# Optimization experiments

Hardware: AMD Instinct MI355X
Metric: run time of the kernel (lower is better)

The kernel has to match this reference:

```python
import jax, jax.numpy as jnp
import numpy as np

B, L, D, H, E, TOP_K = 8, 2048, 1024, 4096, 8, 2
TAU = 1.0
EPS = 1e-9


def setup_inputs() -> dict:
    key = jax.random.key(0)
    ks = jax.random.split(key, 8)
    T = B * L
    s = 0.02
    return {
        "x": jax.random.normal(ks[0], (B, L, D), dtype=jnp.float32),
        "snr": jax.random.uniform(ks[1], (1,), dtype=jnp.float32) * 10.0,
        "gumbel_u": jax.random.uniform(ks[2], (T, E), dtype=jnp.float32),
        "gate_w1": jax.random.normal(ks[3], (D + 1, D), dtype=jnp.float32) * s,
        "gate_b1": jnp.zeros((D,), dtype=jnp.float32),
        "gate_w2": jax.random.normal(ks[4], (D, E), dtype=jnp.float32) * s,
        "gate_b2": jnp.zeros((E,), dtype=jnp.float32),
        "ew1": jax.random.normal(ks[5], (E, D, H), dtype=jnp.float32) * s,
        "eb1": jnp.zeros((E, H), dtype=jnp.float32),
        "ew2": jax.random.normal(ks[6], (E, H, D), dtype=jnp.float32) * s,
        "eb2": jnp.zeros((E, D), dtype=jnp.float32),
    }


def reference(x, snr, gumbel_u, gate_w1, gate_b1, gate_w2, gate_b2, ew1, eb1, ew2, eb2):
    b, l, d = x.shape
    T = b * l
    xf = x.reshape(T, d)  # [T, D]

    # --- gate: Linear(D+1,D) -> ReLU -> Linear(D,E), snr appended per token ---
    g_in = jnp.concatenate([xf, jnp.broadcast_to(snr, (T, 1))], axis=-1)
    h = jax.nn.relu(g_in @ gate_w1 + gate_b1)
    logits = h @ gate_w2 + gate_b2  # [T, E]

    # --- gumbel softmax (soft, hard=False) ---
    gumbel = -jnp.log(-jnp.log(gumbel_u + EPS) + EPS)
    gate_scores = jax.nn.softmax((logits + gumbel) / TAU, axis=-1)  # [T, E]

    # --- top-k dispatch weights ---
    topk_scores, topk_idx = jax.lax.top_k(gate_scores, TOP_K)  # [T, K]
    onehot_k = jax.nn.one_hot(topk_idx, E, dtype=gate_scores.dtype)  # [T, K, E]
    comb = jnp.einsum("tk,tke->te", topk_scores, onehot_k)  # combine weights [T, E]
    expert_mask = onehot_k.sum(axis=1)  # [T, E], 1.0 where expert selected

    # --- per-expert FFN, weighted combine (dense over tokens per expert) ---
    out = jnp.zeros_like(xf)
    for e in range(E):
        he = jax.nn.relu(xf @ ew1[e] + eb1[e])  # [T, H]
        oe = he @ ew2[e] + eb2[e]  # [T, D]
        out = out + comb[:, e:e + 1] * oe

    return out.reshape(b, l, d), gate_scores, expert_mask
```

## Files before the change

kernel.cpp:

```cpp
#include <hip/hip_runtime.h>

typedef unsigned short u16;
typedef __attribute__((ext_vector_type(8))) short bf16x8;
typedef __attribute__((ext_vector_type(4))) float f32x4;

#define T_TOK 16384
#define DDIM  1024
#define HDIM  4096
#define NEXP  8
#define HC    2048

static constexpr size_t XBF_OFF  = 0;
static constexpr size_t EW1T_OFF = XBF_OFF  + (size_t)T_TOK*DDIM*2;
static constexpr size_t EW2T_OFF = EW1T_OFF + (size_t)NEXP*HDIM*DDIM*2;
static constexpr size_t TOK_OFF  = EW2T_OFF + (size_t)NEXP*DDIM*HDIM*2;
static constexpr size_t PICK_OFF = TOK_OFF  + (size_t)NEXP*T_TOK*4;
static constexpr size_t CNT_OFF  = PICK_OFF + (size_t)NEXP*T_TOK*4;
static constexpr size_t BASE_OFF = CNT_OFF  + 256;
static constexpr size_t BEFF_OFF = BASE_OFF + 256;
static constexpr size_t T2S_OFF  = BEFF_OFF + 4096;
static constexpr size_t T2W_OFF  = T2S_OFF  + (size_t)T_TOK*8;
static constexpr size_t OE_OFF   = T2W_OFF  + (size_t)T_TOK*8;
static constexpr size_t OE_ROWS  = 2*T_TOK + 128;
static constexpr size_t HBUF_OFF = OE_OFF + OE_ROWS*(size_t)DDIM*4;
static constexpr size_t WS_NEEDED = HBUF_OFF + OE_ROWS*(size_t)HC*2;
static constexpr size_t XLO_OFF  = HBUF_OFF;
static constexpr size_t W1HT_OFF = XLO_OFF + (size_t)T_TOK*DDIM*2;
static constexpr size_t W1LT_OFF = W1HT_OFF + (size_t)DDIM*DDIM*2;

__device__ __forceinline__ u16 f2bf(float f) {
  unsigned u = __float_as_uint(f);
  unsigned r = (u + 0x7FFFu + ((u >> 16) & 1u)) >> 16;
  return (u16)r;
}
__device__ __forceinline__ float bf2f(u16 b) { return __uint_as_float(((unsigned)b) << 16); }

#define GL16(gp, lp) __builtin_amdgcn_global_load_lds( \
    (const __attribute__((address_space(1))) void*)(gp), \
    (__attribute__((address_space(3))) void*)(lp), 16, 0, 0)

__global__ __launch_bounds__(256) void k_convert_x2(const float* __restrict__ x, u16* __restrict__ xh,
                                                    u16* __restrict__ xl, int n4) {
  int i = blockIdx.x * blockDim.x + threadIdx.x;
  int stride = gridDim.x * blockDim.x;
  for (; i < n4; i += stride) {
    float4 v = *(((const float4*)x) + i);
    u16 h0 = f2bf(v.x), h1 = f2bf(v.y), h2 = f2bf(v.z), h3 = f2bf(v.w);
    u16 l0 = f2bf(v.x - bf2f(h0)), l1 = f2bf(v.y - bf2f(h1));
    u16 l2 = f2bf(v.z - bf2f(h2)), l3 = f2bf(v.w - bf2f(h3));
    uint2 ph, pl;
    ph.x = (unsigned)h0 | ((unsigned)h1 << 16);
    ph.y = (unsigned)h2 | ((unsigned)h3 << 16);
    pl.x = (unsigned)l0 | ((unsigned)l1 << 16);
    pl.y = (unsigned)l2 | ((unsigned)l3 << 16);
    *(uint2*)(xh + (size_t)i * 4) = ph;
    *(uint2*)(xl + (size_t)i * 4) = pl;
  }
}

__global__ __launch_bounds__(256) void k_bias_eff(const float* __restrict__ w1, const float* __restrict__ b1,
                                                  const float* __restrict__ snr, float* __restrict__ beff) {
  int j = blockIdx.x * 256 + threadIdx.x;
  if (j < DDIM) beff[j] = b1[j] + snr[0] * w1[(size_t)DDIM * DDIM + j];
}

__global__ __launch_bounds__(256) void k_transpose_bf16(const float* __restrict__ in, u16* __restrict__ out,
                                                        int Rr, int Cc) {
  __shared__ u16 tile[64][72];
  const float* inE = in + (size_t)blockIdx.z * Rr * Cc;
  u16* outE = out + (size_t)blockIdx.z * Rr * Cc;
  int r0 = blockIdx.x * 64, c0 = blockIdx.y * 64;
  #pragma unroll
  for (int i = 0; i < 4; i++) {
    int id = threadIdx.x + i * 256;
    int r = id >> 4, cq = id & 15;
    float4 v = *(const float4*)(inE + (size_t)(r0 + r) * Cc + c0 + cq * 4);
    tile[cq*4+0][r] = f2bf(v.x);
    tile[cq*4+1][r] = f2bf(v.y);
    tile[cq*4+2][r] = f2bf(v.z);
    tile[cq*4+3][r] = f2bf(v.w);
  }
  __syncthreads();
  #pragma unroll
  for (int i = 0; i < 2; i++) {
    int id = threadIdx.x + i * 256;
    int c = id >> 3, rq = id & 7;
    *(uint4*)(outE + (size_t)(c0 + c) * Rr + r0 + rq * 8) = *(const uint4*)&tile[c][rq * 8];
  }
}

__global__ __launch_bounds__(256) void k_transpose_w1split(const float* __restrict__ w1,
                                                           u16* __restrict__ hT, u16* __restrict__ lT) {
  __shared__ u16 th[64][72];
  __shared__ u16 tl[64][72];
  int r0 = blockIdx.x * 64, c0 = blockIdx.y * 64;
  #pragma unroll
  for (int i = 0; i < 4; i++) {
    int id = threadIdx.x + i * 256;
    int r = id >> 4, cq = id & 15;
    float4 v = *(const float4*)(w1 + (size_t)(r0 + r) * DDIM + c0 + cq * 4);
    u16 h0 = f2bf(v.x), h1 = f2bf(v.y), h2 = f2bf(v.z), h3 = f2bf(v.w);
    th[cq*4+0][r] = h0; tl[cq*4+0][r] = f2bf(v.x - bf2f(h0));
    th[cq*4+1][r] = h1; tl[cq*4+1][r] = f2bf(v.y - bf2f(h1));
    th[cq*4+2][r] = h2; tl[cq*4+2][r] = f2bf(v.z - bf2f(h2));
    th[cq*4+3][r] = h3; tl[cq*4+3][r] = f2bf(v.w - bf2f(h3));
  }
  __syncthreads();
  #pragma unroll
  for (int i = 0; i < 2; i++) {
    int id = threadIdx.x + i * 256;
    int c = id >> 3, rq = id & 7;
    *(uint4*)(hT + (size_t)(c0 + c) * DDIM + r0 + rq * 8) = *(const uint4*)&th[c][rq * 8];
    *(uint4*)(lT + (size_t)(c0 + c) * DDIM + r0 + rq * 8) = *(const uint4*)&tl[c][rq * 8];
  }
}

#define MFMA_STEP(Abuf, Bbuf)                                                     \
  do {                                                                            \
    _Pragma("unroll")                                                             \
    for (int ks = 0; ks < 2; ks++) {                                              \
      const int chk = ks * 4 + (lane >> 4);                                       \
      bf16x8 af[4], bfr[4];                                                       \
      _Pragma("unroll")                                                           \
      for (int m = 0; m < 4; m++) {                                               \
        int row = wr + m * 16 + (lane & 15);                                      \
        af[m] = *(const bf16x8*)&(Abuf)[row * 64 + ((chk ^ (row & 7)) * 8)];      \
      }                                                                           \
      _Pragma("unroll")                                                           \
      for (int n = 0; n < 4; n++) {                                               \
        int col = wc + n * 16 + (lane & 15);                                      \
        bfr[n] = *(const bf16x8*)&(Bbuf)[col * 64 + ((chk ^ (col & 7)) * 8)];     \
      }                                                                           \
      _Pragma("unroll")                                                           \
      for (int m = 0; m < 4; m++)                                                 \
        _Pragma("unroll")                                                         \
        for (int n = 0; n < 4; n++)                                               \
          acc[m][n] = __builtin_amdgcn_mfma_f32_16x16x32_bf16(af[m], bfr[n], acc[m][n], 0, 0, 0); \
    }                                                                             \
  } while (0)

__global__ __launch_bounds__(256) void k_gate_h_mfma(const u16* __restrict__ xh, const u16* __restrict__ xl,
    const u16* __restrict__ w1hT, const u16* __restrict__ w1lT,
    const float* __restrict__ beff, float* __restrict__ h) {
  const int m0 = blockIdx.x * 128, n0 = blockIdx.y * 128;
  __shared__ u16 As[8192];
  __shared__ u16 Bs[8192];
  const int tid = threadIdx.x;
  const int wid = tid >> 6, lane = tid & 63;

  const int cXor = ((lane & 7) ^ (lane >> 3)) * 8;
  size_t aoff[4], boff[4];
  #pragma unroll
  for (int i = 0; i < 4; i++) {
    int seg = wid * 4 + i;
    int rr = seg * 8 + (lane >> 3);
    aoff[i] = (size_t)(m0 + rr) * DDIM + cXor;
    boff[i] = (size_t)(n0 + rr) * DDIM + cXor;
  }
  const u16* Ab[3] = {xh, xh, xl};
  const u16* Bb[3] = {w1hT, w1lT, w1hT};

  const int wr = (wid >> 1) * 64, wc = (wid & 1) * 64;
  f32x4 acc[4][4] = {};

#define STAGE_G(s)                                          \
  do {                                                      \
    const u16* Abase = Ab[(s) >> 4];                        \
    const u16* Bbase = Bb[(s) >> 4];                        \
    const int kt = ((s) & 15) * 64;                         \
    _Pragma("unroll")                                       \
    for (int i = 0; i < 4; i++) {                           \
      int seg = wid * 4 + i;                                \
      GL16(Abase + aoff[i] + kt, &As[seg * 512]);           \
      GL16(Bbase + boff[i] + kt, &Bs[seg * 512]);           \
    }                                                       \
  } while (0)

  STAGE_G(0);
  for (int s = 1; s < 48; s++) {
    __syncthreads();
    MFMA_STEP(As, Bs);
    __syncthreads();
    STAGE_G(s);
  }
  __syncthreads();
  MFMA_STEP(As, Bs);

  #pragma unroll
  for (int m = 0; m < 4; m++) {
    int rt0 = wr + m * 16 + ((lane >> 4) << 2);
    #pragma unroll
    for (int ri = 0; ri < 4; ri++) {
      int row = m0 + rt0 + ri;
      #pragma unroll
      for (int n = 0; n < 4; n++) {
        int col = n0 + wc + n * 16 + (lane & 15);
        h[(size_t)row * DDIM + col] = fmaxf(acc[m][n][ri] + beff[col], 0.f);
      }
    }
  }
#undef STAGE_G
}

__global__ __launch_bounds__(256) void k_gate_logits(const float* __restrict__ h, const float* __restrict__ w2,
    const float* __restrict__ b2, const float* __restrict__ gu, float* __restrict__ scores,
    float* __restrict__ maskp, int* __restrict__ pick, float2* __restrict__ t2w) {
  int wid = threadIdx.x >> 6, lane = threadIdx.x & 63;
  int t = blockIdx.x * 4 + wid;
  const float* hr = h + (size_t)t * DDIM;
  float acc[8] = {0,0,0,0,0,0,0,0};
  for (int kk = 0; kk < DDIM / 64; kk++) {
    int k = kk * 64 + lane;
    float hv = hr[k];
    float4 wa = *(const float4*)(w2 + (size_t)k * 8);
    float4 wb = *(const float4*)(w2 + (size_t)k * 8 + 4);
    acc[0] += hv * wa.x; acc[1] += hv * wa.y; acc[2] += hv * wa.z; acc[3] += hv * wa.w;
    acc[4] += hv * wb.x; acc[5] += hv * wb.y; acc[6] += hv * wb.z; acc[7] += hv * wb.w;
  }
  #pragma unroll
  for (int e = 0; e < 8; e++) {
    #pragma unroll
    for (int off = 32; off > 0; off >>= 1) acc[e] += __shfl_down(acc[e], off);
  }
  if (lane == 0) {
    float sc[8];
    float m = -1e30f;
    #pragma unroll
    for (int e = 0; e < 8; e++) {
      float u = gu[(size_t)t * 8 + e];
      float g = -logf(-logf(u + 1e-9f) + 1e-9f);
      sc[e] = acc[e] + b2[e] + g;
      m = fmaxf(m, sc[e]);
    }
    float s = 0.f;
    #pragma unroll
    for (int e = 0; e < 8; e++) { sc[e] = expf(sc[e] - m); s += sc[e]; }
    float inv = 1.f / s;
    #pragma unroll
    for (int e = 0; e < 8; e++) { sc[e] *= inv; scores[(size_t)t * 8 + e] = sc[e]; }
    int i1 = 0;
    #pragma unroll
    for (int e = 1; e < 8; e++) if (sc[e] > sc[i1]) i1 = e;
    int i2 = (i1 == 0) ? 1 : 0;
    #pragma unroll
    for (int e = 0; e < 8; e++) if (e != i1 && sc[e] > sc[i2]) i2 = e;
    #pragma unroll
    for (int e = 0; e < 8; e++) maskp[(size_t)t * 8 + e] = (e == i1 || e == i2) ? 1.f : 0.f;
    pick[t] = i1 | (i2 << 8);
    t2w[t] = make_float2(sc[i1], sc[i2]);
  }
}

__global__ __launch_bounds__(1024) void k_route(const int* __restrict__ pick,
    int* __restrict__ tokl, int* __restrict__ cnts, int* __restrict__ t2si) {
  const int e = blockIdx.x;
  const int tid = threadIdx.x;
  const int lane = tid & 63, w = tid >> 6;
  __shared__ int wsum[16];
  __shared__ int wbase[16];

  const int t0 = tid * 16;
  int flags = 0, fsel = 0;
  #pragma unroll
  for (int j = 0; j < 16; j++) {
    int p = pick[t0 + j];
    int i1 = p & 0xFF, i2 = (p >> 8) & 0xFF;
    if (i1 == e) { flags |= 1 << j; fsel |= 1 << j; }
    else if (i2 == e) { flags |= 1 << j; }
  }
  int c = __popc(flags);
  int incl = c;
  #pragma unroll
  for (int off = 1; off < 64; off <<= 1) {
    int vv = __shfl_up(incl, off);
    if (lane >= off) incl += vv;
  }
  int waveTotal = __shfl(incl, 63);
  int myExcl = incl - c;
  if (lane == 63) wsum[w] = waveTotal;
  __syncthreads();
  if (tid == 0) {
    int s = 0;
    #pragma unroll
    for (int i = 0; i < 16; i++) { wbase[i] = s; s += wsum[i]; }
    cnts[e] = s;
  }
  __syncthreads();
  int rank = wbase[w] + myExcl;
  #pragma unroll
  for (int j = 0; j < 16; j++) {
    if (flags & (1 << j)) {
      int t = t0 + j;
      tokl[e * T_TOK + rank] = t;
      t2si[2 * t + (((fsel >> j) & 1) ? 0 : 1)] = (e << 16) | rank;
      rank++;
    }
  }
}

__global__ void k_scan(const int* __restrict__ cnts, int* __restrict__ basep) {
  if (threadIdx.x == 0 && blockIdx.x == 0) {
    int s = 0;
    for (int e = 0; e < NEXP; e++) { basep[e] = s; s += cnts[e]; }
  }
}

__global__ __launch_bounds__(256) void k_ffn1(const u16* __restrict__ xbf, const u16* __restrict__ ew1t,
    const float* __restrict__ eb1, const int* __restrict__ tokl, const int* __restrict__ cnts,
    const int* __restrict__ basep, u16* __restrict__ hbuf, int c0) {
  const int e = blockIdx.z;
  const int nt = cnts[e];
  const int r0 = blockIdx.x * 128;
  if (r0 >= nt) return;
  const int hc0 = blockIdx.y * 128;

  __shared__ u16 As[8192];
  __shared__ u16 Bs[8192];
  __shared__ int toks[128];

  const int tid = threadIdx.x;
  const int wid = tid >> 6, lane = tid & 63;
  if (tid < 128) {
    int row = r0 + tid;
    toks[tid] = tokl[e * T_TOK + (row < nt ? row : nt - 1)];
  }
  __syncthreads();

  const int cXor = ((lane & 7) ^ (lane >> 3)) * 8;
  const u16* gA[4];
  const u16* gB[4];
  #pragma unroll
  for (int i = 0; i < 4; i++) {
    int seg = wid * 4 + i;
    int rr = seg * 8 + (lane >> 3);
    gA[i] = xbf + (size_t)toks[rr] * DDIM + cXor;
    gB[i] = ew1t + ((size_t)e * HDIM + c0 + hc0 + rr) * DDIM + cXor;
  }

  const int wr = (wid >> 1) * 64, wc = (wid & 1) * 64;
  f32x4 acc[4][4] = {};

#define STAGE_F1(kt)                                        \
  do {                                                      \
    _Pragma("unroll")                                       \
    for (int i = 0; i < 4; i++) {                           \
      int seg = wid * 4 + i;                                \
      GL16(gA[i] + (kt), &As[seg * 512]);                   \
      GL16(gB[i] + (kt), &Bs[seg * 512]);                   \
    }                                                       \
  } while (0)

  STAGE_F1(0);
  for (int kt = 64; kt < DDIM; kt += 64) {
    __syncthreads();
    MFMA_STEP(As, Bs);
    __syncthreads();
    STAGE_F1(kt);
  }
  __syncthreads();
  MFMA_STEP(As, Bs);

  const int g0 = basep[e];
  #pragma unroll
  for (int m = 0; m < 4; m++) {
    int rt0 = wr + m * 16 + ((lane >> 4) << 2);
    #pragma unroll
    for (int ri = 0; ri < 4; ri++) {
      int rE = r0 + rt0 + ri;
      if (rE < nt) {
        size_t grow = (size_t)(g0 + rE) * HC;
        #pragma unroll
        for (int n = 0; n < 4; n++) {
          int col = hc0 + wc + n * 16 + (lane & 15);
          float v = acc[m][n][ri] + eb1[e * HDIM + c0 + col];
          hbuf[grow + col] = f2bf(fmaxf(v, 0.f));
        }
      }
    }
  }
#undef STAGE_F1
}

__global__ __launch_bounds__(256) void k_ffn2(const u16* __restrict__ hbuf, const u16* __restrict__ ew2t,
    const float* __restrict__ eb2, const int* __restrict__ cnts, const int* __restrict__ basep,
    float* __restrict__ oe, int c0) {
  const int e = blockIdx.z;
  const int nt = cnts[e];
  const int r0 = blockIdx.x * 128;
  if (r0 >= nt) return;
  const int d0 = blockIdx.y * 128;

  __shared__ u16 As[8192];
  __shared__ u16 Bs[8192];

  const int tid = threadIdx.x;
  const int wid = tid >> 6, lane = tid & 63;
  const int g0 = basep[e];

  const int cXor = ((lane & 7) ^ (lane >> 3)) * 8;
  const u16* gA[4];
  const u16* gB[4];
  #pragma unroll
  for (int i = 0; i < 4; i++) {
    int seg = wid * 4 + i;
    int rr = seg * 8 + (lane >> 3);
    int ra = r0 + rr; if (ra >= nt) ra = nt - 1;
    gA[i] = hbuf + (size_t)(g0 + ra) * HC + cXor;
    gB[i] = ew2t + ((size_t)e * DDIM + d0 + rr) * HDIM + c0 + cXor;
  }

  const int wr = (wid >> 1) * 64, wc = (wid & 1) * 64;
  f32x4 acc[4][4] = {};

#define STAGE_F2(kt)                                        \
  do {                                                      \
    _Pragma("unroll")                                       \
    for (int i = 0; i < 4; i++) {                           \
      int seg = wid * 4 + i;                                \
      GL16(gA[i] + (kt), &As[seg * 512]);                   \
      GL16(gB[i] + (kt), &Bs[seg * 512]);                   \
    }                                                       \
  } while (0)

  STAGE_F2(0);
  for (int kt = 64; kt < HC; kt += 64) {
    __syncthreads();
    MFMA_STEP(As, Bs);
    __syncthreads();
    STAGE_F2(kt);
  }
  __syncthreads();
  MFMA_STEP(As, Bs);

  #pragma unroll
  for (int m = 0; m < 4; m++) {
    int rt0 = wr + m * 16 + ((lane >> 4) << 2);
    #pragma unroll
    for (int ri = 0; ri < 4; ri++) {
      int rE = r0 + rt0 + ri;
      if (rE < nt) {
        float* orow = oe + (size_t)(g0 + rE) * DDIM;
        #pragma unroll
        for (int n = 0; n < 4; n++) {
          int col = d0 + wc + n * 16 + (lane & 15);
          float v = acc[m][n][ri];
          if (c0 == 0) orow[col] = v + eb2[e * DDIM + col];
          else         orow[col] += v;
        }
      }
    }
  }
#undef STAGE_F2
}

__global__ __launch_bounds__(256) void k_combine(const float* __restrict__ oe,
    const int2* __restrict__ t2s, const float2* __restrict__ t2w, const int* __restrict__ basep,
    float* __restrict__ out) {
  int wid = threadIdx.x >> 6, lane = threadIdx.x & 63;
  int t = blockIdx.x * 4 + wid;
  int2 s = t2s[t];
  float2 w = t2w[t];
  const float4* pa = (const float4*)(oe + (size_t)(basep[s.x >> 16] + (s.x & 0xFFFF)) * DDIM);
  const float4* pb = (const float4*)(oe + (size_t)(basep[s.y >> 16] + (s.y & 0xFFFF)) * DDIM);
  float4* po = (float4*)(out + (size_t)t * DDIM);
  #pragma unroll
  for (int k = 0; k < 4; k++) {
    int i = k * 64 + lane;
    float4 a = pa[i], b = pb[i];
    float4 o;
    o.x = w.x * a.x + w.y * b.x;
    o.y = w.x * a.y + w.y * b.y;
    o.z = w.x * a.z + w.y * b.z;
    o.w = w.x * a.w + w.y * b.w;
    po[i] = o;
  }
}

extern "C" void kernel_launch(void* const* d_in, const int* in_sizes, int n_in,
                              void* d_out, int out_size, void* d_ws, size_t ws_size,
                              hipStream_t stream) {
  const float* x   = (const float*)d_in[0];
  const float* snr = (const float*)d_in[1];
  const float* gu  = (const float*)d_in[2];
  const float* gw1 = (const float*)d_in[3];
  const float* gb1 = (const float*)d_in[4];
  const float* gw2 = (const float*)d_in[5];
  const float* gb2 = (const float*)d_in[6];
  const float* ew1 = (const float*)d_in[7];
  const float* eb1 = (const float*)d_in[8];
  const float* ew2 = (const float*)d_in[9];
  const float* eb2 = (const float*)d_in[10];

  if (ws_size < WS_NEEDED) return;

  char* ws = (char*)d_ws;
  u16*    xbf   = (u16*)(ws + XBF_OFF);
  u16*    ew1t  = (u16*)(ws + EW1T_OFF);
  u16*    ew2t  = (u16*)(ws + EW2T_OFF);
  int*    tokl  = (int*)(ws + TOK_OFF);
  int*    pick  = (int*)(ws + PICK_OFF);
  int*    cnts  = (int*)(ws + CNT_OFF);
  int*    basep = (int*)(ws + BASE_OFF);
  float*  beff  = (float*)(ws + BEFF_OFF);
  int*    t2si  = (int*)(ws + T2S_OFF);
  int2*   t2s   = (int2*)(ws + T2S_OFF);
  float2* t2w   = (float2*)(ws + T2W_OFF);
  float*  oe    = (float*)(ws + OE_OFF);
  float*  hgate = (float*)(ws + OE_OFF);
  u16*    hbuf  = (u16*)(ws + HBUF_OFF);
  u16*    xlo   = (u16*)(ws + XLO_OFF);
  u16*    w1hT  = (u16*)(ws + W1HT_OFF);
  u16*    w1lT  = (u16*)(ws + W1LT_OFF);

  float* out    = (float*)d_out;
  float* scores = out + (size_t)T_TOK * DDIM;
  float* maskp  = scores + (size_t)T_TOK * NEXP;

  k_convert_x2<<<2048, 256, 0, stream>>>(x, xbf, xlo, T_TOK * DDIM / 4);
  k_bias_eff<<<(DDIM + 255) / 256, 256, 0, stream>>>(gw1, gb1, snr, beff);
  k_transpose_w1split<<<dim3(DDIM / 64, DDIM / 64), 256, 0, stream>>>(gw1, w1hT, w1lT);
  k_transpose_bf16<<<dim3(DDIM / 64, HDIM / 64, NEXP), 256, 0, stream>>>(ew1, ew1t, DDIM, HDIM);
  k_transpose_bf16<<<dim3(HDIM / 64, DDIM / 64, NEXP), 256, 0, stream>>>(ew2, ew2t, HDIM, DDIM);
  k_gate_h_mfma<<<dim3(T_TOK / 128, DDIM / 128), 256, 0, stream>>>(xbf, xlo, w1hT, w1lT, beff, hgate);
  k_gate_logits<<<T_TOK / 4, 256, 0, stream>>>(hgate, gw2, gb2, gu, scores, maskp, pick, t2w);
  k_route<<<NEXP, 1024, 0, stream>>>(pick, tokl, cnts, t2si);
  k_scan<<<1, 64, 0, stream>>>(cnts, basep);

  for (int c = 0; c < HDIM / HC; c++) {
    k_ffn1<<<dim3(T_TOK / 128, HC / 128, NEXP), 256, 0, stream>>>(xbf, ew1t, eb1, tokl, cnts, basep, hbuf, c * HC);
    k_ffn2<<<dim3(T_TOK / 128, DDIM / 128, NEXP), 256, 0, stream>>>(hbuf, ew2t, eb2, cnts, basep, oe, c * HC);
  }
  k_combine<<<T_TOK / 4, 256, 0, stream>>>(oe, t2s, t2w, basep, out);
}
```

Baseline: 1.247 ms.

## Enlarge GEMM tiles to 256x256 with 512 threads and double-buffered LDS pipeline

The three MFMA GEMM kernels (gate hidden, FFN1, FFN2) move from 128x128 tiles with 256 threads to 256x256 tiles with 512 threads. Each wave now computes 128x64. The single LDS buffer with two syncthreads per k-step is replaced by a double-buffered pipeline: the next tile is prefetched with global_load_lds while the current one is computed, using explicit vmcnt waits, s_barrier, sched_barrier and s_setprio around the MFMA block. The aim is more data reuse per LDS load and overlap of global loads with MFMA work. The cost is 128KB of LDS per block and higher register pressure from acc[8][4], which may limit occupancy below the requested two blocks per CU, plus more wasted rows on partial expert tiles. OE_ROWS padding is raised to cover the larger row tiles.

New measurement: 1.794 ms. +43.8%, slower.

```diff
diff --git a/kernel.cpp b/kernel.cpp
--- a/kernel.cpp
+++ b/kernel.cpp
@@ -21,7 +21,7 @@
 static constexpr size_t T2S_OFF  = BEFF_OFF + 4096;
 static constexpr size_t T2W_OFF  = T2S_OFF  + (size_t)T_TOK*8;
 static constexpr size_t OE_OFF   = T2W_OFF  + (size_t)T_TOK*8;
-static constexpr size_t OE_ROWS  = 2*T_TOK + 128;
+static constexpr size_t OE_ROWS  = 2*T_TOK + 256;
 static constexpr size_t HBUF_OFF = OE_OFF + OE_ROWS*(size_t)DDIM*4;
 static constexpr size_t WS_NEEDED = HBUF_OFF + OE_ROWS*(size_t)HC*2;
 static constexpr size_t XLO_OFF  = HBUF_OFF;
@@ -115,36 +115,47 @@
   }
 }
 
-#define MFMA_STEP(Abuf, Bbuf)                                                     \
+#define MFMA_STEP256(Abuf, Bbuf)                                                  \
   do {                                                                            \
     _Pragma("unroll")                                                             \
     for (int ks = 0; ks < 2; ks++) {                                              \
       const int chk = ks * 4 + (lane >> 4);                                       \
-      bf16x8 af[4], bfr[4];                                                       \
+      bf16x8 af[8], bfr[4];                                                       \
       _Pragma("unroll")                                                           \
-      for (int m = 0; m < 4; m++) {                                               \
-        int row = wr + m * 16 + (lane & 15);                                      \
+      for (int m = 0; m < 8; m++) {                                               \
+        int row = wm * 128 + m * 16 + (lane & 15);                                \
         af[m] = *(const bf16x8*)&(Abuf)[row * 64 + ((chk ^ (row & 7)) * 8)];      \
       }                                                                           \
       _Pragma("unroll")                                                           \
       for (int n = 0; n < 4; n++) {                                               \
-        int col = wc + n * 16 + (lane & 15);                                      \
+        int col = wn * 64 + n * 16 + (lane & 15);                                 \
         bfr[n] = *(const bf16x8*)&(Bbuf)[col * 64 + ((chk ^ (col & 7)) * 8)];     \
       }                                                                           \
       _Pragma("unroll")                                                           \
-      for (int m = 0; m < 4; m++)                                                 \
+      for (int m = 0; m < 8; m++)                                                 \
         _Pragma("unroll")                                                         \
         for (int n = 0; n < 4; n++)                                               \
           acc[m][n] = __builtin_amdgcn_mfma_f32_16x16x32_bf16(af[m], bfr[n], acc[m][n], 0, 0, 0); \
     }                                                                             \
   } while (0)
 
-__global__ __launch_bounds__(256) void k_gate_h_mfma(const u16* __restrict__ xh, const u16* __restrict__ xl,
+#define PIPE_BODY(curbuf)                                   \
+  do {                                                      \
+    __builtin_amdgcn_s_barrier();                           \
+    __builtin_amdgcn_sched_barrier(0);                      \
+    __builtin_amdgcn_s_setprio(1);                          \
+    MFMA_STEP256(As[curbuf], Bs[curbuf]);                   \
+    __builtin_amdgcn_s_setprio(0);                          \
+    __builtin_amdgcn_sched_barrier(0);                      \
+    __builtin_amdgcn_s_barrier();                           \
+  } while (0)
+
+__global__ __launch_bounds__(512, 2) void k_gate_h_mfma(const u16* __restrict__ xh, const u16* __restrict__ xl,
     const u16* __restrict__ w1hT, const u16* __restrict__ w1lT,
     const float* __restrict__ beff, float* __restrict__ h) {
-  const int m0 = blockIdx.x * 128, n0 = blockIdx.y * 128;
-  __shared__ u16 As[8192];
-  __shared__ u16 Bs[8192];
+  const int m0 = blockIdx.x * 256, n0 = blockIdx.y * 256;
+  __shared__ u16 As[2][16384];
+  __shared__ u16 Bs[2][16384];
   const int tid = threadIdx.x;
   const int wid = tid >> 6, lane = tid & 63;
 
@@ -152,54 +163,55 @@
   size_t aoff[4], boff[4];
   #pragma unroll
   for (int i = 0; i < 4; i++) {
-    int seg = wid * 4 + i;
-    int rr = seg * 8 + (lane >> 3);
+    int rr = i * 64 + wid * 8 + (lane >> 3);
     aoff[i] = (size_t)(m0 + rr) * DDIM + cXor;
     boff[i] = (size_t)(n0 + rr) * DDIM + cXor;
   }
-  const u16* Ab[3] = {xh, xh, xl};
-  const u16* Bb[3] = {w1hT, w1lT, w1hT};
-
-  const int wr = (wid >> 1) * 64, wc = (wid & 1) * 64;
-  f32x4 acc[4][4] = {};
-
-#define STAGE_G(s)                                          \
+
+  const int wm = wid >> 2, wn = wid & 3;
+  f32x4 acc[8][4] = {};
+
+#define STG_G(t, b)                                         \
   do {                                                      \
-    const u16* Abase = Ab[(s) >> 4];                        \
-    const u16* Bbase = Bb[(s) >> 4];                        \
-    const int kt = ((s) & 15) * 64;                         \
+    const int pass = (t) >> 4;                              \
+    const int kt = ((t) & 15) * 64;                         \
+    const u16* Ab_ = (pass < 2) ? xh : xl;                  \
+    const u16* Bb_ = (pass == 1) ? w1lT : w1hT;             \
     _Pragma("unroll")                                       \
     for (int i = 0; i < 4; i++) {                           \
-      int seg = wid * 4 + i;                                \
-      GL16(Abase + aoff[i] + kt, &As[seg * 512]);           \
-      GL16(Bbase + boff[i] + kt, &Bs[seg * 512]);           \
+      GL16(Ab_ + aoff[i] + kt, &As[b][(i * 64 + wid * 8) * 64]); \
+      GL16(Bb_ + boff[i] + kt, &Bs[b][(i * 64 + wid * 8) * 64]); \
     }                                                       \
   } while (0)
 
-  STAGE_G(0);
-  for (int s = 1; s < 48; s++) {
-    __syncthreads();
-    MFMA_STEP(As, Bs);
-    __syncthreads();
-    STAGE_G(s);
-  }
-  __syncthreads();
-  MFMA_STEP(As, Bs);
-
-  #pragma unroll
-  for (int m = 0; m < 4; m++) {
-    int rt0 = wr + m * 16 + ((lane >> 4) << 2);
+  const int NT = 48;
+  STG_G(0, 0);
+  #pragma unroll 2
+  for (int t = 0; t < NT; t++) {
+    const int cur = t & 1;
+    if (t + 1 < NT) {
+      STG_G(t + 1, cur ^ 1);
+      asm volatile("s_waitcnt vmcnt(8)" ::: "memory");
+    } else {
+      asm volatile("s_waitcnt vmcnt(0)" ::: "memory");
+    }
+    PIPE_BODY(cur);
+  }
+
+  #pragma unroll
+  for (int m = 0; m < 8; m++) {
+    int rt0 = wm * 128 + m * 16 + ((lane >> 4) << 2);
     #pragma unroll
     for (int ri = 0; ri < 4; ri++) {
       int row = m0 + rt0 + ri;
       #pragma unroll
       for (int n = 0; n < 4; n++) {
-        int col = n0 + wc + n * 16 + (lane & 15);
+        int col = n0 + wn * 64 + n * 16 + (lane & 15);
         h[(size_t)row * DDIM + col] = fmaxf(acc[m][n][ri] + beff[col], 0.f);
       }
     }
   }
-#undef STAGE_G
+#undef STG_G
 }
 
 __global__ __launch_bounds__(256) void k_gate_logits(const float* __restrict__ h, const float* __restrict__ w2,
@@ -305,22 +317,22 @@
   }
 }
 
-__global__ __launch_bounds__(256) void k_ffn1(const u16* __restrict__ xbf, const u16* __restrict__ ew1t,
+__global__ __launch_bounds__(512, 2) void k_ffn1(const u16* __restrict__ xbf, const u16* __restrict__ ew1t,
     const float* __restrict__ eb1, const int* __restrict__ tokl, const int* __restrict__ cnts,
     const int* __restrict__ basep, u16* __restrict__ hbuf, int c0) {
   const int e = blockIdx.z;
   const int nt = cnts[e];
-  const int r0 = blockIdx.x * 128;
+  const int r0 = blockIdx.x * 256;
   if (r0 >= nt) return;
-  const int hc0 = blockIdx.y * 128;
-
-  __shared__ u16 As[8192];
-  __shared__ u16 Bs[8192];
-  __shared__ int toks[128];
+  const int hc0 = blockIdx.y * 256;
+
+  __shared__ u16 As[2][16384];
+  __shared__ u16 Bs[2][16384];
+  __shared__ int toks[256];
 
   const int tid = threadIdx.x;
   const int wid = tid >> 6, lane = tid & 63;
-  if (tid < 128) {
+  if (tid < 256) {
     int row = r0 + tid;
     toks[tid] = tokl[e * T_TOK + (row < nt ? row : nt - 1)];
   }
@@ -331,39 +343,42 @@
   const u16* gB[4];
   #pragma unroll
   for (int i = 0; i < 4; i++) {
-    int seg = wid * 4 + i;
-    int rr = seg * 8 + (lane >> 3);
+    int rr = i * 64 + wid * 8 + (lane >> 3);
     gA[i] = xbf + (size_t)toks[rr] * DDIM + cXor;
     gB[i] = ew1t + ((size_t)e * HDIM + c0 + hc0 + rr) * DDIM + cXor;
   }
 
-  const int wr = (wid >> 1) * 64, wc = (wid & 1) * 64;
-  f32x4 acc[4][4] = {};
-
-#define STAGE_F1(kt)                                        \
+  const int wm = wid >> 2, wn = wid & 3;
+  f32x4 acc[8][4] = {};
+
+#define STG_F(t, b)                                         \
   do {                                                      \
+    const int kt = (t) * 64;                                \
     _Pragma("unroll")                                       \
     for (int i = 0; i < 4; i++) {                           \
-      int seg = wid * 4 + i;                                \
-      GL16(gA[i] + (kt), &As[seg * 512]);                   \
-      GL16(gB[i] + (kt), &Bs[seg * 512]);                   \
+      GL16(gA[i] + kt, &As[b][(i * 64 + wid * 8) * 64]);    \
+      GL16(gB[i] + kt, &Bs[b][(i * 64 + wid * 8) * 64]);    \
     }                                                       \
   } while (0)
 
-  STAGE_F1(0);
-  for (int kt = 64; kt < DDIM; kt += 64) {
-    __syncthreads();
-    MFMA_STEP(As, Bs);
-    __syncthreads();
-    STAGE_F1(kt);
-  }
-  __syncthreads();
-  MFMA_STEP(As, Bs);
+  const int NT = DDIM / 64;
+  STG_F(0, 0);
+  #pragma unroll 2
+  for (int t = 0; t < NT; t++) {
+    const int cur = t & 1;
+    if (t + 1 < NT) {
+      STG_F(t + 1, cur ^ 1);
+      asm volatile("s_waitcnt vmcnt(8)" ::: "memory");
+    } else {
+      asm volatile("s_waitcnt vmcnt(0)" ::: "memory");
+    }
+    PIPE_BODY(cur);
+  }
 
   const int g0 = basep[e];
   #pragma unroll
-  for (int m = 0; m < 4; m++) {
-    int rt0 = wr + m * 16 + ((lane >> 4) << 2);
+  for (int m = 0; m < 8; m++) {
+    int rt0 = wm * 128 + m * 16 + ((lane >> 4) << 2);
     #pragma unroll
     for (int ri = 0; ri < 4; ri++) {
       int rE = r0 + rt0 + ri;
@@ -371,27 +386,27 @@
         size_t grow = (size_t)(g0 + rE) * HC;
         #pragma unroll
         for (int n = 0; n < 4; n++) {
-          int col = hc0 + wc + n * 16 + (lane & 15);
+          int col = hc0 + wn * 64 + n * 16 + (lane & 15);
           float v = acc[m][n][ri] + eb1[e * HDIM + c0 + col];
           hbuf[grow + col] = f2bf(fmaxf(v, 0.f));
         }
       }
     }
   }
-#undef STAGE_F1
-}
-
-__global__ __launch_bounds__(256) void k_ffn2(const u16* __restrict__ hbuf, const u16* __restrict__ ew2t,
+#undef STG_F
+}
+
+__global__ __launch_bounds__(512, 2) void k_ffn2(const u16* __restrict__ hbuf, const u16* __restrict__ ew2t,
     const float* __restrict__ eb2, const int* __restrict__ cnts, const int* __restrict__ basep,
     float* __restrict__ oe, int c0) {
   const int e = blockIdx.z;
   const int nt = cnts[e];
-  const int r0 = blockIdx.x * 128;
+  const int r0 = blockIdx.x * 256;
   if (r0 >= nt) return;
-  const int d0 = blockIdx.y * 128;
-
-  __shared__ u16 As[8192];
-  __shared__ u16 Bs[8192];
+  const int d0 = blockIdx.y * 256;
+
+  __shared__ u16 As[2][16384];
+  __shared__ u16 Bs[2][16384];
 
   const int tid = threadIdx.x;
   const int wid = tid >> 6, lane = tid & 63;
@@ -402,39 +417,42 @@
   const u16* gB[4];
   #pragma unroll
   for (int i = 0; i < 4; i++) {
-    int seg = wid * 4 + i;
-    int rr = seg * 8 + (lane >> 3);
+    int rr = i * 64 + wid * 8 + (lane >> 3);
     int ra = r0 + rr; if (ra >= nt) ra = nt - 1;
     gA[i] = hbuf + (size_t)(g0 + ra) * HC + cXor;
     gB[i] = ew2t + ((size_t)e * DDIM + d0 + rr) * HDIM + c0 + cXor;
   }
 
-  const int wr = (wid >> 1) * 64, wc = (wid & 1) * 64;
-  f32x4 acc[4][4] = {};
-
-#define STAGE_F2(kt)                                        \
+  const int wm = wid >> 2, wn = wid & 3;
+  f32x4 acc[8][4] = {};
+
+#define STG_F2(t, b)                                        \
   do {                                                      \
+    const int kt = (t) * 64;                                \
     _Pragma("unroll")                                       \
     for (int i = 0; i < 4; i++) {                           \
-      int seg = wid * 4 + i;                                \
-      GL16(gA[i] + (kt), &As[seg * 512]);                   \
-      GL16(gB[i] + (kt), &Bs[seg * 512]);                   \
+      GL16(gA[i] + kt, &As[b][(i * 64 + wid * 8) * 64]);    \
+      GL16(gB[i] + kt, &Bs[b][(i * 64 + wid * 8) * 64]);    \
     }                                                       \
   } while (0)
 
-  STAGE_F2(0);
-  for (int kt = 64; kt < HC; kt += 64) {
-    __syncthreads();
-    MFMA_STEP(As, Bs);
-    __syncthreads();
-    STAGE_F2(kt);
-  }
-  __syncthreads();
-  MFMA_STEP(As, Bs);
-
-  #pragma unroll
-  for (int m = 0; m < 4; m++) {
-    int rt0 = wr + m * 16 + ((lane >> 4) << 2);
+  const int NT = HC / 64;
+  STG_F2(0, 0);
+  #pragma unroll 2
+  for (int t = 0; t < NT; t++) {
+    const int cur = t & 1;
+    if (t + 1 < NT) {
+      STG_F2(t + 1, cur ^ 1);
+      asm volatile("s_waitcnt vmcnt(8)" ::: "memory");
+    } else {
+      asm volatile("s_waitcnt vmcnt(0)" ::: "memory");
+    }
+    PIPE_BODY(cur);
+  }
+
+  #pragma unroll
+  for (int m = 0; m < 8; m++) {
+    int rt0 = wm * 128 + m * 16 + ((lane >> 4) << 2);
     #pragma unroll
     for (int ri = 0; ri < 4; ri++) {
       int rE = r0 + rt0 + ri;
@@ -442,7 +460,7 @@
         float* orow = oe + (size_t)(g0 + rE) * DDIM;
         #pragma unroll
         for (int n = 0; n < 4; n++) {
-          int col = d0 + wc + n * 16 + (lane & 15);
+          int col = d0 + wn * 64 + n * 16 + (lane & 15);
           float v = acc[m][n][ri];
           if (c0 == 0) orow[col] = v + eb2[e * DDIM + col];
           else         orow[col] += v;
@@ -450,7 +468,7 @@
       }
     }
   }
-#undef STAGE_F2
+#undef STG_F2
 }
 
 __global__ __launch_bounds__(256) void k_combine(const float* __restrict__ oe,
@@ -521,14 +539,14 @@
   k_transpose_w1split<<<dim3(DDIM / 64, DDIM / 64), 256, 0, stream>>>(gw1, w1hT, w1lT);
   k_transpose_bf16<<<dim3(DDIM / 64, HDIM / 64, NEXP), 256, 0, stream>>>(ew1, ew1t, DDIM, HDIM);
   k_transpose_bf16<<<dim3(HDIM / 64, DDIM / 64, NEXP), 256, 0, stream>>>(ew2, ew2t, HDIM, DDIM);
-  k_gate_h_mfma<<<dim3(T_TOK / 128, DDIM / 128), 256, 0, stream>>>(xbf, xlo, w1hT, w1lT, beff, hgate);
+  k_gate_h_mfma<<<dim3(T_TOK / 256, DDIM / 256), 512, 0, stream>>>(xbf, xlo, w1hT, w1lT, beff, hgate);
   k_gate_logits<<<T_TOK / 4, 256, 0, stream>>>(hgate, gw2, gb2, gu, scores, maskp, pick, t2w);
   k_route<<<NEXP, 1024, 0, stream>>>(pick, tokl, cnts, t2si);
   k_scan<<<1, 64, 0, stream>>>(cnts, basep);
 
   for (int c = 0; c < HDIM / HC; c++) {
-    k_ffn1<<<dim3(T_TOK / 128, HC / 128, NEXP), 256, 0, stream>>>(xbf, ew1t, eb1, tokl, cnts, basep, hbuf, c * HC);
-    k_ffn2<<<dim3(T_TOK / 128, DDIM / 128, NEXP), 256, 0, stream>>>(hbuf, ew2t, eb2, cnts, basep, oe, c * HC);
+    k_ffn1<<<dim3(T_TOK / 256, HC / 256, NEXP), 512, 0, stream>>>(xbf, ew1t, eb1, tokl, cnts, basep, hbuf, c * HC);
+    k_ffn2<<<dim3(T_TOK / 256, DDIM / 256, NEXP), 512, 0, stream>>>(hbuf, ew2t, eb2, cnts, basep, oe, c * HC);
   }
   k_combine<<<T_TOK / 4, 256, 0, stream>>>(oe, t2s, t2w, basep, out);
 }
```

## Pipeline ffn2 with four-stage K=32 LDS ring and persistent row loops

Applied to the files above, without the earlier changes.

The second expert GEMM now loads K in 32-wide slices into a four-buffer LDS ring. Loads run three stages ahead, controlled by explicit vmcnt waits and raw barriers, so global loads overlap MFMA work instead of alternating with it. Both FFN kernels also become grid-stride over token tiles with a fixed 40-block x-dimension, which avoids launching many empty blocks for experts with few tokens. The cost is finer-grained barriers in ffn2 and a possible load imbalance when an expert has more tiles than the grid covers.

After: 1.778 ms. +42.6%, slower.

```diff
diff --git a/kernel.cpp b/kernel.cpp
--- a/kernel.cpp
+++ b/kernel.cpp
@@ -21,7 +21,7 @@
 static constexpr size_t T2S_OFF  = BEFF_OFF + 4096;
 static constexpr size_t T2W_OFF  = T2S_OFF  + (size_t)T_TOK*8;
 static constexpr size_t OE_OFF   = T2W_OFF  + (size_t)T_TOK*8;
-static constexpr size_t OE_ROWS  = 2*T_TOK + 128;
+static constexpr size_t OE_ROWS  = 2*T_TOK + 256;
 static constexpr size_t HBUF_OFF = OE_OFF + OE_ROWS*(size_t)DDIM*4;
 static constexpr size_t WS_NEEDED = HBUF_OFF + OE_ROWS*(size_t)HC*2;
 static constexpr size_t XLO_OFF  = HBUF_OFF;
@@ -139,6 +139,28 @@
     }                                                                             \
   } while (0)
 
+#define SW32(r) ((((r) & 3) ^ (((r) >> 2) & 3)))
+#define MFMA_STEP32(Abuf, Bbuf)                                                   \
+  do {                                                                            \
+    const int chk = lane >> 4;                                                    \
+    bf16x8 af[4], bfr[4];                                                         \
+    _Pragma("unroll")                                                             \
+    for (int m = 0; m < 4; m++) {                                                 \
+      int row = wr + m * 16 + (lane & 15);                                        \
+      af[m] = *(const bf16x8*)&(Abuf)[row * 32 + ((chk ^ SW32(row)) * 8)];        \
+    }                                                                             \
+    _Pragma("unroll")                                                             \
+    for (int n = 0; n < 4; n++) {                                                 \
+      int col = wc + n * 16 + (lane & 15);                                        \
+      bfr[n] = *(const bf16x8*)&(Bbuf)[col * 32 + ((chk ^ SW32(col)) * 8)];       \
+    }                                                                             \
+    _Pragma("unroll")                                                             \
+    for (int m = 0; m < 4; m++)                                                   \
+      _Pragma("unroll")                                                           \
+      for (int n = 0; n < 4; n++)                                                 \
+        acc[m][n] = __builtin_amdgcn_mfma_f32_16x16x32_bf16(af[m], bfr[n], acc[m][n], 0, 0, 0); \
+  } while (0)
+
 __global__ __launch_bounds__(256) void k_gate_h_mfma(const u16* __restrict__ xh, const u16* __restrict__ xl,
     const u16* __restrict__ w1hT, const u16* __restrict__ w1lT,
     const float* __restrict__ beff, float* __restrict__ h) {
@@ -310,9 +332,8 @@
     const int* __restrict__ basep, u16* __restrict__ hbuf, int c0) {
   const int e = blockIdx.z;
   const int nt = cnts[e];
-  const int r0 = blockIdx.x * 128;
-  if (r0 >= nt) return;
   const int hc0 = blockIdx.y * 128;
+  const int g0 = basep[e];
 
   __shared__ u16 As[8192];
   __shared__ u16 Bs[8192];
@@ -320,65 +341,68 @@
 
   const int tid = threadIdx.x;
   const int wid = tid >> 6, lane = tid & 63;
-  if (tid < 128) {
-    int row = r0 + tid;
-    toks[tid] = tokl[e * T_TOK + (row < nt ? row : nt - 1)];
-  }
-  __syncthreads();
-
   const int cXor = ((lane & 7) ^ (lane >> 3)) * 8;
-  const u16* gA[4];
-  const u16* gB[4];
-  #pragma unroll
-  for (int i = 0; i < 4; i++) {
-    int seg = wid * 4 + i;
-    int rr = seg * 8 + (lane >> 3);
-    gA[i] = xbf + (size_t)toks[rr] * DDIM + cXor;
-    gB[i] = ew1t + ((size_t)e * HDIM + c0 + hc0 + rr) * DDIM + cXor;
-  }
-
   const int wr = (wid >> 1) * 64, wc = (wid & 1) * 64;
-  f32x4 acc[4][4] = {};
+
+  for (int r0 = blockIdx.x * 128; r0 < nt; r0 += gridDim.x * 128) {
+    __syncthreads();
+    if (tid < 128) {
+      int row = r0 + tid;
+      toks[tid] = tokl[e * T_TOK + (row < nt ? row : nt - 1)];
+    }
+    __syncthreads();
+
+    const u16* gA[4];
+    const u16* gB[4];
+    #pragma unroll
+    for (int i = 0; i < 4; i++) {
+      int seg = wid * 4 + i;
+      int rr = seg * 8 + (lane >> 3);
+      gA[i] = xbf + (size_t)toks[rr] * DDIM + cXor;
+      gB[i] = ew1t + ((size_t)e * HDIM + c0 + hc0 + rr) * DDIM + cXor;
+    }
+
+    f32x4 acc[4][4] = {};
 
 #define STAGE_F1(kt)                                        \
-  do {                                                      \
-    _Pragma("unroll")                                       \
-    for (int i = 0; i < 4; i++) {                           \
-      int seg = wid * 4 + i;                                \
-      GL16(gA[i] + (kt), &As[seg * 512]);                   \
-      GL16(gB[i] + (kt), &Bs[seg * 512]);                   \
-    }                                                       \
-  } while (0)
-
-  STAGE_F1(0);
-  for (int kt = 64; kt < DDIM; kt += 64) {
+    do {                                                    \
+      _Pragma("unroll")                                     \
+      for (int i = 0; i < 4; i++) {                         \
+        int seg = wid * 4 + i;                              \
+        GL16(gA[i] + (kt), &As[seg * 512]);                 \
+        GL16(gB[i] + (kt), &Bs[seg * 512]);                 \
+      }                                                     \
+    } while (0)
+
+    STAGE_F1(0);
+    for (int kt = 64; kt < DDIM; kt += 64) {
+      __syncthreads();
+      MFMA_STEP(As, Bs);
+      __syncthreads();
+      STAGE_F1(kt);
+    }
     __syncthreads();
     MFMA_STEP(As, Bs);
-    __syncthreads();
-    STAGE_F1(kt);
-  }
-  __syncthreads();
-  MFMA_STEP(As, Bs);
-
-  const int g0 = basep[e];
-  #pragma unroll
-  for (int m = 0; m < 4; m++) {
-    int rt0 = wr + m * 16 + ((lane >> 4) << 2);
-    #pragma unroll
-    for (int ri = 0; ri < 4; ri++) {
-      int rE = r0 + rt0 + ri;
-      if (rE < nt) {
-        size_t grow = (size_t)(g0 + rE) * HC;
-        #pragma unroll
-        for (int n = 0; n < 4; n++) {
-          int col = hc0 + wc + n * 16 + (lane & 15);
-          float v = acc[m][n][ri] + eb1[e * HDIM + c0 + col];
-          hbuf[grow + col] = f2bf(fmaxf(v, 0.f));
+
+    #pragma unroll
+    for (int m = 0; m < 4; m++) {
+      int rt0 = wr + m * 16 + ((lane >> 4) << 2);
+      #pragma unroll
+      for (int ri = 0; ri < 4; ri++) {
+        int rE = r0 + rt0 + ri;
+        if (rE < nt) {
+          size_t grow = (size_t)(g0 + rE) * HC;
+          #pragma unroll
+          for (int n = 0; n < 4; n++) {
+            int col = hc0 + wc + n * 16 + (lane & 15);
+            float v = acc[m][n][ri] + eb1[e * HDIM + c0 + col];
+            hbuf[grow + col] = f2bf(fmaxf(v, 0.f));
+          }
         }
       }
     }
-  }
 #undef STAGE_F1
+  }
 }
 
 __global__ __launch_bounds__(256) void k_ffn2(const u16* __restrict__ hbuf, const u16* __restrict__ ew2t,
@@ -386,71 +410,82 @@
     float* __restrict__ oe, int c0) {
   const int e = blockIdx.z;
   const int nt = cnts[e];
-  const int r0 = blockIdx.x * 128;
-  if (r0 >= nt) return;
   const int d0 = blockIdx.y * 128;
-
-  __shared__ u16 As[8192];
-  __shared__ u16 Bs[8192];
+  const int g0 = basep[e];
+
+  __shared__ u16 As[4][4096];
+  __shared__ u16 Bs[4][4096];
 
   const int tid = threadIdx.x;
   const int wid = tid >> 6, lane = tid & 63;
-  const int g0 = basep[e];
-
-  const int cXor = ((lane & 7) ^ (lane >> 3)) * 8;
-  const u16* gA[4];
-  const u16* gB[4];
-  #pragma unroll
-  for (int i = 0; i < 4; i++) {
-    int seg = wid * 4 + i;
-    int rr = seg * 8 + (lane >> 3);
-    int ra = r0 + rr; if (ra >= nt) ra = nt - 1;
-    gA[i] = hbuf + (size_t)(g0 + ra) * HC + cXor;
-    gB[i] = ew2t + ((size_t)e * DDIM + d0 + rr) * HDIM + c0 + cXor;
-  }
-
   const int wr = (wid >> 1) * 64, wc = (wid & 1) * 64;
-  f32x4 acc[4][4] = {};
-
-#define STAGE_F2(kt)                                        \
-  do {                                                      \
-    _Pragma("unroll")                                       \
-    for (int i = 0; i < 4; i++) {                           \
-      int seg = wid * 4 + i;                                \
-      GL16(gA[i] + (kt), &As[seg * 512]);                   \
-      GL16(gB[i] + (kt), &Bs[seg * 512]);                   \
-    }                                                       \
-  } while (0)
-
-  STAGE_F2(0);
-  for (int kt = 64; kt < HC; kt += 64) {
+  const int cXor32 = (((lane & 3) ^ ((lane >> 2) & 3) ^ ((lane >> 4) & 3))) * 8;
+  const int NT32 = HC / 32;
+
+  for (int r0 = blockIdx.x * 128; r0 < nt; r0 += gridDim.x * 128) {
     __syncthreads();
-    MFMA_STEP(As, Bs);
-    __syncthreads();
-    STAGE_F2(kt);
-  }
-  __syncthreads();
-  MFMA_STEP(As, Bs);
-
-  #pragma unroll
-  for (int m = 0; m < 4; m++) {
-    int rt0 = wr + m * 16 + ((lane >> 4) << 2);
-    #pragma unroll
-    for (int ri = 0; ri < 4; ri++) {
-      int rE = r0 + rt0 + ri;
-      if (rE < nt) {
-        float* orow = oe + (size_t)(g0 + rE) * DDIM;
-        #pragma unroll
-        for (int n = 0; n < 4; n++) {
-          int col = d0 + wc + n * 16 + (lane & 15);
-          float v = acc[m][n][ri];
-          if (c0 == 0) orow[col] = v + eb2[e * DDIM + col];
-          else         orow[col] += v;
+
+    const u16* gA[2];
+    const u16* gB[2];
+    #pragma unroll
+    for (int i = 0; i < 2; i++) {
+      int rr = (wid * 2 + i) * 16 + (lane >> 2);
+      int ra = r0 + rr; if (ra >= nt) ra = nt - 1;
+      gA[i] = hbuf + (size_t)(g0 + ra) * HC + cXor32;
+      gB[i] = ew2t + ((size_t)e * DDIM + d0 + rr) * HDIM + c0 + cXor32;
+    }
+
+    f32x4 acc[4][4] = {};
+
+#define STAGE32_F2(kt, b)                                   \
+    do {                                                    \
+      _Pragma("unroll")                                     \
+      for (int i = 0; i < 2; i++) {                         \
+        int seg = wid * 2 + i;                              \
+        GL16(gA[i] + (kt), &As[b][seg * 512]);              \
+        GL16(gB[i] + (kt), &Bs[b][seg * 512]);              \
+      }                                                     \
+    } while (0)
+
+    STAGE32_F2(0, 0);
+    STAGE32_F2(32, 1);
+    STAGE32_F2(64, 2);
+    asm volatile("s_waitcnt vmcnt(8)" ::: "memory");
+    __builtin_amdgcn_s_barrier();
+
+    #pragma unroll 4
+    for (int t = 0; t < NT32; t++) {
+      const int b = t & 3;
+      if (t + 3 < NT32) STAGE32_F2((t + 3) * 32, (t + 3) & 3);
+      MFMA_STEP32(As[b], Bs[b]);
+      if (t + 1 < NT32) {
+        if (t + 3 < NT32)      asm volatile("s_waitcnt vmcnt(8)" ::: "memory");
+        else if (t + 2 < NT32) asm volatile("s_waitcnt vmcnt(4)" ::: "memory");
+        else                   asm volatile("s_waitcnt vmcnt(0)" ::: "memory");
+        __builtin_amdgcn_s_barrier();
+      }
+    }
+#undef STAGE32_F2
+
+    #pragma unroll
+    for (int m = 0; m < 4; m++) {
+      int rt0 = wr + m * 16 + ((lane >> 4) << 2);
+      #pragma unroll
+      for (int ri = 0; ri < 4; ri++) {
+        int rE = r0 + rt0 + ri;
+        if (rE < nt) {
+          float* orow = oe + (size_t)(g0 + rE) * DDIM;
+          #pragma unroll
+          for (int n = 0; n < 4; n++) {
+            int col = d0 + wc + n * 16 + (lane & 15);
+            float v = acc[m][n][ri];
+            if (c0 == 0) orow[col] = v + eb2[e * DDIM + col];
+            else         orow[col] += v;
+          }
         }
       }
     }
   }
-#undef STAGE_F2
 }
 
 __global__ __launch_bounds__(256) void k_combine(const float* __restrict__ oe,
@@ -527,8 +562,8 @@
   k_scan<<<1, 64, 0, stream>>>(cnts, basep);
 
   for (int c = 0; c < HDIM / HC; c++) {
-    k_ffn1<<<dim3(T_TOK / 128, HC / 128, NEXP), 256, 0, stream>>>(xbf, ew1t, eb1, tokl, cnts, basep, hbuf, c * HC);
-    k_ffn2<<<dim3(T_TOK / 128, DDIM / 128, NEXP), 256, 0, stream>>>(hbuf, ew2t, eb2, cnts, basep, oe, c * HC);
+    k_ffn1<<<dim3(40, HC / 128, NEXP), 256, 0, stream>>>(xbf, ew1t, eb1, tokl, cnts, basep, hbuf, c * HC);
+    k_ffn2<<<dim3(40, DDIM / 128, NEXP), 256, 0, stream>>>(hbuf, ew2t, eb2, cnts, basep, oe, c * HC);
   }
   k_combine<<<T_TOK / 4, 256, 0, stream>>>(oe, t2s, t2w, basep, out);
 }
```
